# Optimization experiments

Hardware: AMD Instinct MI355X
Metric: run time of the kernel (lower is better)

Reference implementation:

```python
import jax, jax.numpy as jnp
import numpy as np
from jax import lax

BIN_NUM = 48
CPG = BIN_NUM * 3            # 144 hidden channels
NOUT = BIN_NUM + 1           # 49 symbols
K = 5                        # masked conv kernel size
H, W = 256, 512
TABLE_TOTAL = 65536.0        # EntropyTable total frequency
SCALE = 2.0 / (BIN_NUM - 1.0)


def _causal_mask(include_center: bool) -> jnp.ndarray:
    # Raster-scan causal 5x5 mask: all rows above center, left of center in
    # center row; center tap only for 'hidden' (mask-B) layers.
    m = np.zeros((K, K), np.float32)
    c = K // 2
    m[:c, :] = 1.0
    m[c, :c] = 1.0
    if include_center:
        m[c, c] = 1.0
    return jnp.asarray(m)[None, None]  # broadcast over (O, I, kh, kw)


def _mconv(x, w, b, mask):
    # x: (N, C, H, W); w: (O, I, K, K)
    y = lax.conv_general_dilated(
        x, w * mask, window_strides=(1, 1), padding='SAME',
        dimension_numbers=('NCHW', 'OIHW', 'NCHW'))
    return y + b[None, :, None, None]


def setup_inputs() -> dict:
    key = jax.random.key(0)
    ks = jax.random.split(key, 8)
    # quantized code indices in [0, BIN_NUM)
    data = jax.random.randint(ks[0], (1, 1, H, W), 0, BIN_NUM).astype(jnp.float32)
    s0 = 1.0 / np.sqrt(1 * K * K)
    sr = 1.0 / np.sqrt(CPG * K * K)
    w0 = jax.random.normal(ks[1], (CPG, 1, K, K), jnp.float32) * s0
    b0 = jnp.zeros((CPG,), jnp.float32)
    # 5 residual blocks x 2 convs = 10 hidden masked convs, stacked
    wres = jax.random.normal(ks[2], (10, CPG, CPG, K, K), jnp.float32) * sr
    bres = jnp.zeros((10, CPG), jnp.float32)
    wl = jax.random.normal(ks[3], (NOUT, CPG, K, K), jnp.float32) * sr
    bl = jnp.zeros((NOUT,), jnp.float32)
    return {"data": data, "w0": w0, "b0": b0, "wres": wres, "bres": bres,
            "wl": wl, "bl": bl}


def reference(data, w0, b0, wres, bres, wl, bl):
    mask_a = _causal_mask(False)   # first layer excludes center pixel
    mask_b = _causal_mask(True)    # hidden layers include center pixel

    # Scale(-1, 2/(bin_num-1)): map codes [0, bin_num-1] -> [-1, 1]
    x = data * SCALE - 1.0
    x = jax.nn.relu(_mconv(x, w0, b0, mask_a))
    # 5 residual blocks: y = relu(conv(relu(conv(x)))) + x
    for i in range(5):
        h1 = jax.nn.relu(_mconv(x, wres[2 * i], bres[2 * i], mask_b))
        h2 = jax.nn.relu(_mconv(h1, wres[2 * i + 1], bres[2 * i + 1], mask_b))
        x = x + h2
    logits = _mconv(x, wl, bl, mask_b)          # (1, 49, H, W)

    # EntropyTable: per-pixel softmax -> cumulative frequency table (total 65536)
    probs = jax.nn.softmax(logits, axis=1)
    cdf = jnp.cumsum(probs, axis=1) * TABLE_TOTAL
    zeros = jnp.zeros((cdf.shape[0], 1) + cdf.shape[2:], cdf.dtype)
    vec = jnp.concatenate([zeros, cdf], axis=1)  # (1, 50, H, W)
    return vec
```

## Files before the change

kernel.cpp:

```cpp
#include <hip/hip_runtime.h>

#define HH 256
#define WW 512
#define CPG 144
#define NKG 18
#define WP 516
#define HPADR 258
#define XB_E ((size_t)NKG * HPADR * WP * 8)
#define NCH 59
#define KREAL 1872
#define SCALE_F (2.0f / 47.0f)

typedef __attribute__((ext_vector_type(8))) short short8;
typedef __attribute__((ext_vector_type(4))) float floatx4;

__device__ __forceinline__ unsigned short f2bf(float f) {
    unsigned u = __builtin_bit_cast(unsigned, f);
    u += 0x7FFFu + ((u >> 16) & 1u);
    return (unsigned short)(u >> 16);
}
__device__ __forceinline__ float bf2f(unsigned short h) {
    unsigned u = ((unsigned)h) << 16;
    return __builtin_bit_cast(float, u);
}
__device__ __forceinline__ void async16(const void* g, void* l) {
    __builtin_amdgcn_global_load_lds(
        (const __attribute__((address_space(1))) unsigned int*)g,
        (__attribute__((address_space(3))) unsigned int*)l, 16, 0, 0);
}
__device__ __forceinline__ void tap_decode(int t, int& kh, int& kw) {
    kh = t < 5 ? 0 : (t < 10 ? 1 : 2);
    kw = t - (t < 5 ? 0 : (t < 10 ? 5 : 10));
}

__global__ void k_zero(float* __restrict__ p, size_t n4) {
    size_t i = (size_t)blockIdx.x * blockDim.x + threadIdx.x;
    size_t stride = (size_t)gridDim.x * blockDim.x;
    float4 z = make_float4(0.f, 0.f, 0.f, 0.f);
    for (; i < n4; i += stride) ((float4*)p)[i] = z;
}

__global__ void k_pack_hidden(const float* __restrict__ wres, unsigned short* __restrict__ wpk) {
    const int total = 10 * NCH * CPG * 32;
    int i = blockIdx.x * blockDim.x + threadIdx.x;
    int stride = gridDim.x * blockDim.x;
    for (; i < total; i += stride) {
        int kk = i & 31;
        int q  = i >> 5;
        int co = q % CPG;
        int c  = (q / CPG) % NCH;
        int l  = q / (CPG * NCH);
        int K = c * 32 + kk;
        float v = 0.f;
        if (K < KREAL) {
            int t = K / CPG, ci = K - t * CPG;
            int kh, kw; tap_decode(t, kh, kw);
            v = wres[(((size_t)(l * CPG + co) * CPG + ci) * 5 + kh) * 5 + kw];
        }
        wpk[i] = f2bf(v);
    }
}
__global__ void k_pack_final(const float* __restrict__ wl, unsigned short* __restrict__ wpkF) {
    const int total = NCH * 64 * 32;
    int i = blockIdx.x * blockDim.x + threadIdx.x;
    if (i >= total) return;
    int kk = i & 31;
    int co = (i >> 5) & 63;
    int c  = i >> 11;
    int K = c * 32 + kk;
    float v = 0.f;
    if (K < KREAL && co < 49) {
        int t = K / CPG, ci = K - t * CPG;
        int kh, kw; tap_decode(t, kh, kw);
        v = wl[(((size_t)co * CPG + ci) * 5 + kh) * 5 + kw];
    }
    wpkF[i] = f2bf(v);
}
__global__ void k_pack_small(const float* __restrict__ w0, const float* __restrict__ bl,
                             float* __restrict__ w0p, float* __restrict__ blp) {
    int i = blockIdx.x * blockDim.x + threadIdx.x;
    if (i < 12 * CPG) {
        int co = i % CPG, t = i / CPG;
        int kh, kw; tap_decode(t, kh, kw);
        w0p[i] = w0[co * 25 + kh * 5 + kw];
    } else if (i < 12 * CPG + 64) {
        int k = i - 12 * CPG;
        blp[k] = k < 49 ? bl[k] : 0.f;
    }
}

__global__ __launch_bounds__(384) void k_layer0(
    const float* __restrict__ data, const float* __restrict__ w0p,
    const float* __restrict__ b0, unsigned short* __restrict__ Xb) {
    const int lane = threadIdx.x;
    const int x = blockIdx.x * 64 + lane;
    const int y = blockIdx.y;

    float xv[12];
#pragma unroll
    for (int t = 0; t < 12; t++) {
        int kh, kw; tap_decode(t, kh, kw);
        int yy = y + kh - 2, xx = x + kw - 2;
        xv[t] = (yy >= 0 && xx >= 0 && xx < WW) ? data[yy * WW + xx] * SCALE_F - 1.0f : 0.f;
    }
#pragma unroll
    for (int kgi = 0; kgi < 3; kgi++) {
        int kg = threadIdx.y * 3 + kgi;
        float a8[8];
#pragma unroll
        for (int j = 0; j < 8; j++) a8[j] = 0.f;
#pragma unroll
        for (int t = 0; t < 12; t++)
#pragma unroll
            for (int j = 0; j < 8; j++)
                a8[j] = fmaf(w0p[t * CPG + kg * 8 + j], xv[t], a8[j]);
        short8 o;
#pragma unroll
        for (int j = 0; j < 8; j++)
            o[j] = (short)f2bf(fmaxf(a8[j] + b0[kg * 8 + j], 0.f));
        *(short8*)&Xb[((size_t)(kg * HPADR + y + 2) * WP + (x + 2)) * 8] = o;
    }
}

template<bool RES>
__global__ __launch_bounds__(768, 3) void k_conv(
    const unsigned short* __restrict__ in,
    const unsigned short* __restrict__ wq,
    const float* __restrict__ bias,
    const unsigned short* __restrict__ res,
    unsigned short* __restrict__ out) {
    __shared__ __align__(16) unsigned short As[NKG][4][132][8];
    const int tid  = threadIdx.x;
    const int lane = tid & 63;
    const int wid  = tid >> 6;
    const int ng   = wid % 3;
    const int r    = (wid / 3) & 1;
    const int ph   = wid / 6;
    const int lr = lane & 15;
    const int lg = lane >> 4;

    const int fid = blockIdx.x + (int)gridDim.x * blockIdx.y;
    const int swz = (fid & 7) * 64 + (fid >> 3);
    const int x0 = (swz & 3) * 128;
    const int y0 = (swz >> 2) * 2;

    floatx4 acc[4][3];
#pragma unroll
    for (int m = 0; m < 4; m++)
#pragma unroll
        for (int n = 0; n < 3; n++) acc[m][n] = (floatx4)0.f;

    auto stage_rows = [&](int r0) {
        for (int i = wid; i < 72; i += 12) {
            int kg = i >> 2;
            int rr = r0 + ((i >> 1) & 1);
            int half = i & 1;
            async16(in + ((size_t)(kg * HPADR + y0 + rr) * WP + x0 + half * 64 + lane) * 8,
                    &As[kg][rr][half * 64][0]);
        }
    };

    auto LDA = [&](int c, short8 (&a)[4]) {
        int g = c * 4 + lg;
        if (g > 233) g = 233;
        int t = (g * 57) >> 10;
        int kgp = g - t * 18;
        int kh, kw; tap_decode(t, kh, kw);
        const unsigned short* ap = &As[kgp][r + kh][ph * 64 + kw + lr][0];
#pragma unroll
        for (int m = 0; m < 4; ++m) a[m] = *(const short8*)(ap + m * 16 * 8);
    };
    auto LDB = [&](int c, short8 (&b)[3]) {
        const unsigned short* bp = wq + (size_t)c * 4608 + (ng * 48 + lr) * 32 + lg * 8;
#pragma unroll
        for (int n = 0; n < 3; ++n) b[n] = *(const short8*)(bp + n * 512);
    };
    auto CMP = [&](const short8 (&a)[4], const short8 (&b)[3]) {
#pragma unroll
        for (int m = 0; m < 4; ++m)
#pragma unroll
            for (int n = 0; n < 3; ++n)
                acc[m][n] = __builtin_amdgcn_mfma_f32_16x16x32_bf16(a[m], b[n], acc[m][n], 0, 0, 0);
    };

    stage_rows(0);
    if (tid < 288) {
        int kg = tid >> 4;
        int rr = (tid >> 2) & 3;
        int pxl = 128 + (tid & 3);
        *(short8*)&As[kg][rr][pxl][0] =
            *(const short8*)(in + ((size_t)(kg * HPADR + y0 + rr) * WP + x0 + pxl) * 8);
    }
    asm volatile("s_waitcnt vmcnt(0) lgkmcnt(0)" ::: "memory");
    __builtin_amdgcn_s_barrier();
    __builtin_amdgcn_sched_barrier(0);
    stage_rows(2);

    short8 a0[4], b0_[3], a1[4], b1_[3];
    LDA(0, a0); LDB(0, b0_);
#pragma unroll 1
    for (int c = 0; c < 20; c += 2) {
        LDA(c + 1, a1); LDB(c + 1, b1_);
        CMP(a0, b0_);
        LDA(c + 2, a0); LDB(c + 2, b0_);
        CMP(a1, b1_);
    }
    LDA(21, a1); LDB(21, b1_);
    CMP(a0, b0_);
    CMP(a1, b1_);
    asm volatile("s_waitcnt vmcnt(0)" ::: "memory");
    __builtin_amdgcn_s_barrier();
    __builtin_amdgcn_sched_barrier(0);

    LDA(22, a0); LDB(22, b0_);
#pragma unroll 1
    for (int c = 22; c + 2 <= 58; c += 2) {
        LDA(c + 1, a1); LDB(c + 1, b1_);
        CMP(a0, b0_);
        LDA(c + 2, a0); LDB(c + 2, b0_);
        CMP(a1, b1_);
    }
    CMP(a0, b0_);

#pragma unroll
    for (int n = 0; n < 3; ++n) {
        int co = ng * 48 + n * 16 + lr;
        float bv = bias[co];
        const size_t pb = ((size_t)((co >> 3) * HPADR + y0 + 2 + r) * WP + (x0 + 2)) * 8 + (co & 7);
#pragma unroll
        for (int m = 0; m < 4; ++m)
#pragma unroll
            for (int rr = 0; rr < 4; ++rr) {
                int px = ph * 64 + m * 16 + lg * 4 + rr;
                size_t o = pb + (size_t)px * 8;
                float v = fmaxf(acc[m][n][rr] + bv, 0.f);
                if (RES) v += bf2f(res[o]);
                out[o] = f2bf(v);
            }
    }
}

__global__ __launch_bounds__(256, 2) void k_logits(
    const unsigned short* __restrict__ in,
    const unsigned short* __restrict__ wq,
    const float* __restrict__ blp,
    float* __restrict__ logits) {
    const int lane = threadIdx.x & 63;
    const int wid  = threadIdx.x >> 6;
    const int lr = lane & 15;
    const int lg = lane >> 4;
    const int tt = blockIdx.x * 4 + wid;
    const int y  = tt >> 2;
    const int x0 = (tt & 3) * 128;

    floatx4 acc[8][4];
#pragma unroll
    for (int m = 0; m < 8; m++)
#pragma unroll
        for (int n = 0; n < 4; n++) acc[m][n] = (floatx4)0.f;

#pragma unroll 1
    for (int c = 0; c < NCH; ++c) {
        int g = c * 4 + lg;
        if (g > 233) g = 233;
        int t = (g * 57) >> 10;
        int kgp = g - t * 18;
        int kh, kw; tap_decode(t, kh, kw);
        const unsigned short* ap =
            in + ((size_t)(kgp * HPADR + y + kh) * WP + (x0 + kw + lr)) * 8;
        const unsigned short* bp =
            wq + ((size_t)c * 64 + lr) * 32 + lg * 8;
        short8 a[8], b[4];
#pragma unroll
        for (int m = 0; m < 8; ++m) a[m] = *(const short8*)(ap + m * 128);
#pragma unroll
        for (int n = 0; n < 4; ++n) b[n] = *(const short8*)(bp + n * 512);
#pragma unroll
        for (int m = 0; m < 8; ++m)
#pragma unroll
            for (int n = 0; n < 4; ++n)
                acc[m][n] = __builtin_amdgcn_mfma_f32_16x16x32_bf16(
                    a[m], b[n], acc[m][n], 0, 0, 0);
    }

#pragma unroll
    for (int n = 0; n < 4; ++n) {
        int co = n * 16 + lr;
        float bv = blp[co];
#pragma unroll
        for (int m = 0; m < 8; ++m)
#pragma unroll
            for (int rr = 0; rr < 4; ++rr) {
                int px = m * 16 + lg * 4 + rr;
                logits[((size_t)y * WW + x0 + px) * 64 + co] = acc[m][n][rr] + bv;
            }
    }
}

__global__ __launch_bounds__(256) void k_softmax(
    const float* __restrict__ lg, float* __restrict__ out) {
    const int px = blockIdx.x * 256 + threadIdx.x;
    const int y = blockIdx.y;
    const size_t p = (size_t)y * WW + px;
    const float* l = lg + p * 64;
    float v[49];
    float m = -1e30f;
#pragma unroll
    for (int k = 0; k < 49; k++) { v[k] = l[k]; m = fmaxf(m, v[k]); }
    float s = 0.f;
#pragma unroll
    for (int k = 0; k < 49; k++) {
        v[k] = exp2f((v[k] - m) * 1.44269504088896f);
        s += v[k];
    }
    const float inv = 65536.0f / s;
    out[p] = 0.f;
    float run = 0.f;
#pragma unroll
    for (int k = 0; k < 49; k++) {
        run += v[k];
        out[(size_t)(k + 1) * (HH * WW) + p] = run * inv;
    }
}

extern "C" void kernel_launch(void* const* d_in, const int* in_sizes, int n_in,
                              void* d_out, int out_size, void* d_ws, size_t ws_size,
                              hipStream_t stream) {
    (void)in_sizes; (void)n_in; (void)out_size; (void)ws_size;
    const float* data = (const float*)d_in[0];
    const float* w0   = (const float*)d_in[1];
    const float* b0   = (const float*)d_in[2];
    const float* wres = (const float*)d_in[3];
    const float* bres = (const float*)d_in[4];
    const float* wl   = (const float*)d_in[5];
    const float* bl   = (const float*)d_in[6];
    float* out = (float*)d_out;

    char* ws = (char*)d_ws;
    unsigned short* Xb   = (unsigned short*)ws;
    unsigned short* Hb   = Xb + XB_E;
    unsigned short* wpk  = Hb + XB_E;
    unsigned short* wpkF = wpk + (size_t)10 * NCH * CPG * 32;
    float* blp  = (float*)(wpkF + (size_t)NCH * 64 * 32);
    float* w0p  = blp + 64;
    float* logits = w0p + 1728;

    k_zero<<<2048, 256, 0, stream>>>((float*)ws, (2 * XB_E * 2) / 16);

    k_pack_hidden<<<2048, 256, 0, stream>>>(wres, wpk);
    k_pack_final<<<(NCH * 64 * 32 + 255) / 256, 256, 0, stream>>>(wl, wpkF);
    k_pack_small<<<7, 256, 0, stream>>>(w0, bl, w0p, blp);

    k_layer0<<<dim3(8, 256), dim3(64, 6), 0, stream>>>(data, w0p, b0, Xb);

    const size_t LSTRIDE = (size_t)NCH * CPG * 32;
    for (int i = 0; i < 5; i++) {
        k_conv<false><<<dim3(4, 128), 768, 0, stream>>>(
            Xb, wpk + (size_t)(2 * i) * LSTRIDE, bres + (2 * i) * CPG, Xb, Hb);
        k_conv<true><<<dim3(4, 128), 768, 0, stream>>>(
            Hb, wpk + (size_t)(2 * i + 1) * LSTRIDE, bres + (2 * i + 1) * CPG, Xb, Xb);
    }

    k_logits<<<256, 256, 0, stream>>>(Xb, wpkF, blp, logits);
    k_softmax<<<dim3(2, 256), 256, 0, stream>>>(logits, out);
}
```

Before: 983.6 us.

## Stage all input rows upfront and precompute tap offsets in LDS table

After: 977.1 us. Within noise of the previous version (-0.7%).

```diff
diff --git a/kernel.cpp b/kernel.cpp
--- a/kernel.cpp
+++ b/kernel.cpp
@@ -130,6 +130,7 @@
     const unsigned short* __restrict__ res,
     unsigned short* __restrict__ out) {
     __shared__ __align__(16) unsigned short As[NKG][4][132][8];
+    __shared__ unsigned toff[NCH][4];
     const int tid  = threadIdx.x;
     const int lane = tid & 63;
     const int wid  = tid >> 6;
@@ -150,40 +151,13 @@
 #pragma unroll
         for (int n = 0; n < 3; n++) acc[m][n] = (floatx4)0.f;
 
-    auto stage_rows = [&](int r0) {
-        for (int i = wid; i < 72; i += 12) {
-            int kg = i >> 2;
-            int rr = r0 + ((i >> 1) & 1);
-            int half = i & 1;
-            async16(in + ((size_t)(kg * HPADR + y0 + rr) * WP + x0 + half * 64 + lane) * 8,
-                    &As[kg][rr][half * 64][0]);
-        }
-    };
-
-    auto LDA = [&](int c, short8 (&a)[4]) {
-        int g = c * 4 + lg;
-        if (g > 233) g = 233;
-        int t = (g * 57) >> 10;
-        int kgp = g - t * 18;
-        int kh, kw; tap_decode(t, kh, kw);
-        const unsigned short* ap = &As[kgp][r + kh][ph * 64 + kw + lr][0];
-#pragma unroll
-        for (int m = 0; m < 4; ++m) a[m] = *(const short8*)(ap + m * 16 * 8);
-    };
-    auto LDB = [&](int c, short8 (&b)[3]) {
-        const unsigned short* bp = wq + (size_t)c * 4608 + (ng * 48 + lr) * 32 + lg * 8;
-#pragma unroll
-        for (int n = 0; n < 3; ++n) b[n] = *(const short8*)(bp + n * 512);
-    };
-    auto CMP = [&](const short8 (&a)[4], const short8 (&b)[3]) {
-#pragma unroll
-        for (int m = 0; m < 4; ++m)
-#pragma unroll
-            for (int n = 0; n < 3; ++n)
-                acc[m][n] = __builtin_amdgcn_mfma_f32_16x16x32_bf16(a[m], b[n], acc[m][n], 0, 0, 0);
-    };
-
-    stage_rows(0);
+    for (int i = wid; i < 144; i += 12) {
+        int half = i & 1;
+        int rr   = (i >> 1) & 3;
+        int kg   = i >> 3;
+        async16(in + ((size_t)(kg * HPADR + y0 + rr) * WP + x0 + half * 64 + lane) * 8,
+                &As[kg][rr][half * 64][0]);
+    }
     if (tid < 288) {
         int kg = tid >> 4;
         int rr = (tid >> 2) & 3;
@@ -191,33 +165,45 @@
         *(short8*)&As[kg][rr][pxl][0] =
             *(const short8*)(in + ((size_t)(kg * HPADR + y0 + rr) * WP + x0 + pxl) * 8);
     }
+    if (tid < NCH * 4) {
+        int c = tid >> 2, l2 = tid & 3;
+        int g = c * 4 + l2;
+        if (g > 233) g = 233;
+        int t = (g * 57) >> 10;
+        int kgp = g - t * 18;
+        int kh, kw; tap_decode(t, kh, kw);
+        toff[c][l2] = (unsigned)(((kgp * 4 + kh) * 132 + kw) * 16);
+    }
     asm volatile("s_waitcnt vmcnt(0) lgkmcnt(0)" ::: "memory");
     __builtin_amdgcn_s_barrier();
     __builtin_amdgcn_sched_barrier(0);
-    stage_rows(2);
+
+    const char* abase = (const char*)&As[0][r][ph * 64 + lr][0];
+    auto LDA = [&](int c, short8 (&a)[4]) {
+        const unsigned short* ap = (const unsigned short*)(abase + toff[c][lg]);
+#pragma unroll
+        for (int m = 0; m < 4; ++m) a[m] = *(const short8*)(ap + m * 16 * 8);
+    };
+    auto LDB = [&](int c, short8 (&b)[3]) {
+        const unsigned short* bp = wq + (size_t)c * 4608 + (ng * 48 + lr) * 32 + lg * 8;
+#pragma unroll
+        for (int n = 0; n < 3; ++n) b[n] = *(const short8*)(bp + n * 512);
+    };
+    auto CMP = [&](const short8 (&a)[4], const short8 (&b)[3]) {
+#pragma unroll
+        for (int m = 0; m < 4; ++m)
+#pragma unroll
+            for (int n = 0; n < 3; ++n)
+                acc[m][n] = __builtin_amdgcn_mfma_f32_16x16x32_bf16(a[m], b[n], acc[m][n], 0, 0, 0);
+    };
 
     short8 a0[4], b0_[3], a1[4], b1_[3];
-    LDA(0, a0); LDB(0, b0_);
+    LDB(0, b0_); LDA(0, a0);
 #pragma unroll 1
-    for (int c = 0; c < 20; c += 2) {
-        LDA(c + 1, a1); LDB(c + 1, b1_);
+    for (int c = 0; c < 58; c += 2) {
+        LDB(c + 1, b1_); LDA(c + 1, a1);
         CMP(a0, b0_);
-        LDA(c + 2, a0); LDB(c + 2, b0_);
-        CMP(a1, b1_);
-    }
-    LDA(21, a1); LDB(21, b1_);
-    CMP(a0, b0_);
-    CMP(a1, b1_);
-    asm volatile("s_waitcnt vmcnt(0)" ::: "memory");
-    __builtin_amdgcn_s_barrier();
-    __builtin_amdgcn_sched_barrier(0);
-
-    LDA(22, a0); LDB(22, b0_);
-#pragma unroll 1
-    for (int c = 22; c + 2 <= 58; c += 2) {
-        LDA(c + 1, a1); LDB(c + 1, b1_);
-        CMP(a0, b0_);
-        LDA(c + 2, a0); LDB(c + 2, b0_);
+        LDB(c + 2, b0_); LDA(c + 2, a0);
         CMP(a1, b1_);
     }
     CMP(a0, b0_);
```
